# Kernel optimization log

Measured on AMD Instinct MI355X. Metric: run time of the kernel, lower is better.

The kernel has to match this reference:

```python
import jax, jax.numpy as jnp
import numpy as np

C = 256
RED = 8
CR = C // RED  # 32
B, H, W = 4, 64, 64
EPS = 1e-5


def setup_inputs() -> dict:
    key = jax.random.key(0)
    ks = jax.random.split(key, 12)
    s = 0.05
    return {
        "x": jax.random.normal(ks[0], (B, C, H, W), dtype=jnp.float32),
        "Wq": jax.random.normal(ks[1], (CR, C), dtype=jnp.float32) * s,
        "bq": jax.random.normal(ks[2], (CR,), dtype=jnp.float32) * s,
        "Wk": jax.random.normal(ks[3], (CR, C), dtype=jnp.float32) * s,
        "bk": jax.random.normal(ks[4], (CR,), dtype=jnp.float32) * s,
        "Wv": jax.random.normal(ks[5], (C, C), dtype=jnp.float32) * s,
        "bv": jax.random.normal(ks[6], (C,), dtype=jnp.float32) * s,
        "Wo": jax.random.normal(ks[7], (C, C), dtype=jnp.float32) * s,
        "bo": jax.random.normal(ks[8], (C,), dtype=jnp.float32) * s,
        "gamma": jnp.ones((C,), dtype=jnp.float32),
        "beta": jnp.zeros((C,), dtype=jnp.float32),
        "running_mean": jax.random.normal(ks[9], (C,), dtype=jnp.float32) * s,
        "running_var": jax.random.uniform(ks[10], (C,), dtype=jnp.float32, minval=0.5, maxval=1.5),
    }


def reference(x, Wq, bq, Wk, bk, Wv, bv, Wo, bo, gamma, beta, running_mean, running_var):
    b, c, h, w = x.shape
    n = h * w
    scale = c ** (-0.5)  # use_scale=True: in_channels**-0.5
    xf = x.reshape(b, c, n)  # [B, C, N]
    # 1x1 convs == per-pixel channel matmuls
    q = jnp.einsum('oc,bcn->bon', Wq, xf) + bq[None, :, None]   # [B, CR, N]
    k = jnp.einsum('oc,bcn->bon', Wk, xf) + bk[None, :, None]   # [B, CR, N]
    v = jnp.einsum('oc,bcn->bon', Wv, xf) + bv[None, :, None]   # [B, C, N]
    # attention[b, q_pos, k_pos], softmax over key positions (dim=2)
    attn = jnp.einsum('bcq,bck->bqk', q, k) * scale             # [B, N, N]
    attn = jax.nn.softmax(attn, axis=2)
    # out[b, c, q_pos] = sum_k v[b, c, k] * attn[b, q_pos, k]
    out = jnp.einsum('bck,bqk->bcq', v, attn)                   # [B, C, N]
    out = jnp.einsum('oc,bcn->bon', Wo, out) + bo[None, :, None]
    # BatchNorm2d (inference: running stats)
    inv = gamma / jnp.sqrt(running_var + EPS)
    out = out * inv[None, :, None] + (beta - running_mean * inv)[None, :, None]
    out = out.reshape(b, c, h, w)
    return jax.nn.relu(out + x)
```

## Files before the change

kernel.cpp:

```cpp
#include <hip/hip_runtime.h>
#include <hip/hip_bf16.h>

typedef unsigned short u16;
typedef unsigned int u32;

#define B_ 4
#define C_ 256
#define N_ 4096

constexpr float C1 = 0.09016844005556021f;

typedef float f32x16 __attribute__((ext_vector_type(16)));
typedef short bf16x8 __attribute__((ext_vector_type(8)));
typedef u32 u32x4 __attribute__((ext_vector_type(4)));
typedef int i32x2 __attribute__((ext_vector_type(2)));

__device__ __forceinline__ u16 bf16r(float f) {
    union { float f; u32 u; } a; a.f = f;
    u32 u = a.u;
    u += 0x7fffu + ((u >> 16) & 1u);
    return (u16)(u >> 16);
}

__device__ __forceinline__ float bf2f(u16 h) {
    union { u32 u; float f; } a; a.u = ((u32)h) << 16; return a.f;
}

__device__ __forceinline__ u32 pk2(float a, float b) {
    __hip_bfloat162 h = __float22bfloat162_rn(make_float2(a, b));
    union { __hip_bfloat162 h; u32 u; } c; c.h = h;
    return c.u;
}

__device__ __forceinline__ u32 cvtpk(float lo, float hi) {
    u32 r;
    asm("v_cvt_pk_bf16_f32 %0, %1, %2" : "=v"(r) : "v"(lo), "v"(hi));
    return r;
}

__device__ __forceinline__ void swap32(u32 &a, u32 &b) {
#if __has_builtin(__builtin_amdgcn_permlane32_swap)
    i32x2 r = __builtin_amdgcn_permlane32_swap((int)a, (int)b, false, false);
    a = (u32)r.x; b = (u32)r.y;
#else
    u32 as = __shfl_xor(a, 32), bs = __shfl_xor(b, 32);
    int hi = (threadIdx.x & 32) ? 1 : 0;
    u32 na = hi ? bs : a;
    u32 nb = hi ? b : as;
    a = na; b = nb;
#endif
}

__device__ __forceinline__ bf16x8 ld8(const u16* p) {
    return *reinterpret_cast<const bf16x8*>(p);
}

__device__ __forceinline__ void gld_lds16(const u16* g, u16* lbase, int lane) {
#if __has_builtin(__builtin_amdgcn_global_load_lds)
    __builtin_amdgcn_global_load_lds(
        (const __attribute__((address_space(1))) void*)g,
        (__attribute__((address_space(3))) void*)lbase, 16, 0, 0);
#else
    *reinterpret_cast<bf16x8*>(lbase + lane * 8) = ld8(g);
#endif
}

__device__ __forceinline__ int crow(int r, int hi) { return (r & 3) + 8 * (r >> 2) + 4 * hi; }

__global__ __launch_bounds__(256) void prep(
    const float* __restrict__ Wq, const float* __restrict__ Wk,
    const float* __restrict__ Wv, const float* __restrict__ Wo,
    const float* __restrict__ bo, const float* __restrict__ gamma,
    const float* __restrict__ beta, const float* __restrict__ rm, const float* __restrict__ rv,
    u16* __restrict__ wqk, u16* __restrict__ wv_b, u16* __restrict__ wo_b,
    float* __restrict__ scale, float* __restrict__ shift)
{
    int i = blockIdx.x * 256 + threadIdx.x;
    if (i < 16384) {
        float w = (i < 8192) ? Wq[i] * C1 : Wk[i - 8192];
        wqk[i] = bf16r(w);
    } else if (i < 81920) {
        wv_b[i - 16384] = bf16r(Wv[i - 16384]);
    } else if (i < 147456) {
        wo_b[i - 81920] = bf16r(Wo[i - 81920]);
    } else if (i < 147712) {
        int o = i - 147456;
        float inv = gamma[o] * rsqrtf(rv[o] + 1e-5f);
        scale[o] = inv;
        shift[o] = beta[o] + (bo[o] - rm[o]) * inv;
    }
}

__global__ __launch_bounds__(512) void projf(
    const float* __restrict__ x, const u16* __restrict__ wqk, const u16* __restrict__ wv,
    const float* __restrict__ bq, const float* __restrict__ bk, const float* __restrict__ bv,
    u16* __restrict__ qkt, u16* __restrict__ vout)
{
    __shared__ u16 xt[64 * 256];
    int tid = threadIdx.x;
    int lane = tid & 63, wid = tid >> 6;
    int r31 = lane & 31, hi = lane >> 5;
    int b = blockIdx.y, n0 = blockIdx.x * 64;
    const float* xb = x + (size_t)b * C_ * N_ + n0;
#pragma unroll
    for (int i = 0; i < 16; ++i) {
        int c2 = i * 8 + wid;
        int n = lane;
        float a0 = xb[(size_t)(2 * c2) * N_ + n];
        float a1 = xb[(size_t)(2 * c2 + 1) * N_ + n];
        int slot = (c2 >> 2) ^ (n & 31);
        *reinterpret_cast<u32*>(&xt[n * 256 + slot * 8 + (c2 & 3) * 2]) = pk2(a0, a1);
    }
    __syncthreads();
    for (int i = 0; i < 3; ++i) {
        int t = wid + i * 8;
        if (t < 20) {
            bool isqk = (t < 4);
            int nb = isqk ? (t >> 1) * 32 : ((t - 4) & 1) * 32;
            int gb = isqk ? (t & 1) * 32 : ((t - 4) >> 1) * 32;
            const u16* grow = (isqk ? wqk : wv) + (size_t)(gb + r31) * C_ + hi * 8;
            f32x16 acc;
#pragma unroll
            for (int r = 0; r < 16; ++r) acc[r] = 0.f;
#pragma unroll
            for (int ks = 0; ks < 16; ++ks) {
                int slot = (2 * ks + hi) ^ r31;
                bf16x8 lf = ld8(&xt[(nb + r31) * 256 + slot * 8]);
                bf16x8 gf = ld8(grow + ks * 16);
                if (isqk) acc = __builtin_amdgcn_mfma_f32_32x32x16_bf16(lf, gf, acc, 0, 0, 0);
                else      acc = __builtin_amdgcn_mfma_f32_32x32x16_bf16(gf, lf, acc, 0, 0, 0);
            }
            if (isqk) {
                int o = gb + r31;
                float bias = (o < 32) ? bq[o] * C1 : bk[o - 32];
                u16* qrow = qkt + ((size_t)b * N_ + n0 + nb) * 64 + o;
#pragma unroll
                for (int r = 0; r < 16; ++r)
                    qrow[(size_t)crow(r, hi) * 64] = bf16r(acc[r] + bias);
            } else {
                u16* vb = vout + (size_t)b * C_ * N_ + n0 + nb + r31;
#pragma unroll
                for (int r = 0; r < 16; ++r) {
                    int c = gb + crow(r, hi);
                    vb[(size_t)c * N_] = bf16r(acc[r] + bv[c]);
                }
            }
        }
    }
}

__global__ __launch_bounds__(512, 4) void attn(
    const u16* __restrict__ qkt, const u16* __restrict__ v,
    u16* __restrict__ opart, float* __restrict__ lpart, int kts)
{
    __shared__ u16 vt[2][128 * 128];
    __shared__ u16 ktt[2][16 * 128];
    int tid = threadIdx.x;
    int lane = tid & 63, wid = tid >> 6;
    int r31 = lane & 31, hi = lane >> 5;

    int nwg = 32 * 4 * gridDim.z;
    int wgl = blockIdx.x + 32 * (blockIdx.y + 4 * blockIdx.z);
    int cpx = nwg >> 3;
    int swzid = (wgl & 7) * cpx + (wgl >> 3);
    int bx = swzid & 31;
    int by = (swzid >> 5) & 3;
    int bz = swzid >> 7;

    int b = by, zs = bz;
    int q0 = bx * 128 + (wid >> 1) * 32;
    int cb = (wid & 1) * 128;
    const u16* qkb = qkt + (size_t)b * N_ * 64;
    const u16* vbase = v + (size_t)b * C_ * N_;

    int ks_q = tid & 255;
    int ks_row = ks_q >> 4;
    int ks_so = (ks_q & 15) ^ ks_row;
    int ks_k = ks_row * 4 + (ks_so >> 2);
    int ks_d8 = (ks_so & 3) * 8;

    int cpar8 = ((cb + r31) & 1) * 8;
    int vrow0 = (cb + r31) >> 1;
    int vm = vrow0 & 15;
    int kr4 = r31 >> 2;
    int kk3 = (r31 & 3) * 4;

    bf16x8 qf0 = ld8(qkb + (size_t)(q0 + r31) * 64 + hi * 8);
    bf16x8 qf1 = ld8(qkb + (size_t)(q0 + r31) * 64 + 16 + hi * 8);

    f32x16 acc[4];
#pragma unroll
    for (int ct = 0; ct < 4; ++ct)
#pragma unroll
        for (int r = 0; r < 16; ++r) acc[ct][r] = 0.f;

    f32x16 z4;
#pragma unroll
    for (int r = 0; r < 16; ++r) z4[r] = 0.f;

    float l_run = 0.f;
    int ktBeg = zs * kts, ktEnd = (zs + 1) * kts;

    auto stage = [&](int buf, int kt) {
        int k0 = kt * 64;
        if (tid < 256)
            gld_lds16(qkb + (size_t)(k0 + ks_k) * 64 + 32 + ks_d8,
                      &ktt[buf][(size_t)(wid * 64) * 8], lane);
#pragma unroll
        for (int i = 0; i < 4; ++i) {
            int q = i * 512 + tid;
            int row2 = q >> 4;
            int so = (q & 15) ^ (row2 & 15);
            int c = 2 * row2 + (so >> 3);
            int kcol = (so & 7) * 8;
            gld_lds16(vbase + (size_t)c * N_ + k0 + kcol,
                      &vt[buf][(size_t)((i * 512 + wid * 64) * 8)], lane);
        }
    };

    int cur = 0;
    stage(cur, ktBeg);
    __syncthreads();

    for (int kt = ktBeg; kt < ktEnd; ++kt) {
        if (kt + 1 < ktEnd) stage(cur ^ 1, kt + 1);

        float pst = 0.f;
#pragma unroll
        for (int ph = 0; ph < 2; ++ph) {
            int krow = ph * 8 + kr4;
            const u16* kbase = &ktt[cur][krow * 128];
            bf16x8 kf0 = ld8(kbase + (((kk3 + hi) ^ krow) * 8));
            bf16x8 kf1 = ld8(kbase + (((kk3 + 2 + hi) ^ krow) * 8));
            f32x16 s = __builtin_amdgcn_mfma_f32_32x32x16_bf16(kf0, qf0, z4, 0, 0, 0);
            s = __builtin_amdgcn_mfma_f32_32x32x16_bf16(kf1, qf1, s, 0, 0, 0);
            float p[16];
#pragma unroll
            for (int r = 0; r < 16; ++r) { p[r] = __builtin_amdgcn_exp2f(s[r]); pst += p[r]; }
            bf16x8 pf[2];
#pragma unroll
            for (int c16 = 0; c16 < 2; ++c16) {
                u32 w0 = cvtpk(p[8 * c16 + 0], p[8 * c16 + 1]);
                u32 w1 = cvtpk(p[8 * c16 + 2], p[8 * c16 + 3]);
                u32 w2 = cvtpk(p[8 * c16 + 4], p[8 * c16 + 5]);
                u32 w3 = cvtpk(p[8 * c16 + 6], p[8 * c16 + 7]);
                swap32(w0, w2);
                swap32(w1, w3);
                union { bf16x8 f8; u32 u[4]; } fu;
                fu.u[0] = w0; fu.u[1] = w1; fu.u[2] = w2; fu.u[3] = w3;
                pf[c16] = fu.f8;
            }
            int kc0 = ph * 2;
#pragma unroll
            for (int ct = 0; ct < 4; ++ct) {
                const u16* vb2 = &vt[cur][(vrow0 + 16 * ct) * 128];
                bf16x8 vf0 = ld8(vb2 + (((cpar8 + kc0 * 2 + hi) ^ vm) * 8));
                bf16x8 vf1 = ld8(vb2 + (((cpar8 + kc0 * 2 + 2 + hi) ^ vm) * 8));
                acc[ct] = __builtin_amdgcn_mfma_f32_32x32x16_bf16(vf0, pf[0], acc[ct], 0, 0, 0);
                acc[ct] = __builtin_amdgcn_mfma_f32_32x32x16_bf16(vf1, pf[1], acc[ct], 0, 0, 0);
            }
        }
        pst += __shfl_xor(pst, 32);
        l_run += pst;

        __syncthreads();
        cur ^= 1;
    }

    u16* dst = opart + ((size_t)(zs * B_ + b) * N_) * C_;
    if ((wid & 1) == 0 && hi == 0)
        lpart[((size_t)zs * B_ + b) * N_ + q0 + r31] = l_run;
    float (*tls)[32][33] = reinterpret_cast<float (*)[32][33]>(&vt[0][0]);
    int qg = lane >> 4, cd = lane & 15;
#pragma unroll
    for (int ct = 0; ct < 4; ++ct) {
        __syncthreads();
#pragma unroll
        for (int r = 0; r < 16; ++r)
            tls[wid][crow(r, hi)][r31] = acc[ct][r];
        __syncthreads();
#pragma unroll
        for (int it = 0; it < 8; ++it) {
            int qp = it * 4 + qg;
            u32 w = pk2(tls[wid][2 * cd][qp], tls[wid][2 * cd + 1][qp]);
            *reinterpret_cast<u32*>(dst + (size_t)(q0 + qp) * C_ + cb + ct * 32 + 2 * cd) = w;
        }
    }
}

__global__ __launch_bounds__(512) void outprojf(
    const u16* __restrict__ opart, const float* __restrict__ lpart,
    const u16* __restrict__ wo, const float* __restrict__ scl, const float* __restrict__ shf,
    const float* __restrict__ x, float* __restrict__ out, int S)
{
    __shared__ u16 ot[64 * 256];
    __shared__ float linv[64];
    int tid = threadIdx.x;
    int lane = tid & 63, wid = tid >> 6;
    int r31 = lane & 31, hi = lane >> 5;
    int b = blockIdx.y, n0 = blockIdx.x * 64;
    if (tid < 64) {
        float l = 0.f;
        for (int s = 0; s < S; ++s) l += lpart[((size_t)s * B_ + b) * N_ + n0 + tid];
        linv[tid] = 1.f / l;
    }
    __syncthreads();
#pragma unroll
    for (int i = 0; i < 4; ++i) {
        int chunk = i * 512 + tid;
        int n = chunk >> 5, c8 = chunk & 31;
        float a[8];
#pragma unroll
        for (int j = 0; j < 8; ++j) a[j] = 0.f;
        for (int s = 0; s < S; ++s) {
            bf16x8 o = ld8(opart + (((size_t)s * B_ + b) * N_ + n0 + n) * C_ + c8 * 8);
#pragma unroll
            for (int j = 0; j < 8; ++j) a[j] += bf2f((u16)o[j]);
        }
        float li = linv[n];
        u32x4 w;
#pragma unroll
        for (int j = 0; j < 4; ++j) w[j] = pk2(a[2 * j] * li, a[2 * j + 1] * li);
        int sws = c8 ^ (n & 31);
        *reinterpret_cast<u32x4*>(&ot[n * 256 + sws * 8]) = w;
    }
    __syncthreads();
    int obs = wid * 32;
    const u16* arow = wo + (size_t)(obs + r31) * C_ + hi * 8;
    f32x16 acc0, acc1;
#pragma unroll
    for (int r = 0; r < 16; ++r) { acc0[r] = 0.f; acc1[r] = 0.f; }
#pragma unroll
    for (int ks = 0; ks < 16; ++ks) {
        bf16x8 af = ld8(arow + ks * 16);
        int slot = (2 * ks + hi) ^ r31;
        bf16x8 b0 = ld8(&ot[r31 * 256 + slot * 8]);
        bf16x8 b1 = ld8(&ot[(32 + r31) * 256 + slot * 8]);
        acc0 = __builtin_amdgcn_mfma_f32_32x32x16_bf16(af, b0, acc0, 0, 0, 0);
        acc1 = __builtin_amdgcn_mfma_f32_32x32x16_bf16(af, b1, acc1, 0, 0, 0);
    }
    const float* xb = x + (size_t)b * C_ * N_;
    float* op = out + (size_t)b * C_ * N_;
#pragma unroll
    for (int r = 0; r < 16; ++r) {
        int o = obs + crow(r, hi);
        float sc = scl[o], sh = shf[o];
        size_t base = (size_t)o * N_ + n0;
        float v0 = acc0[r] * sc + sh + xb[base + r31];
        op[base + r31] = fmaxf(v0, 0.f);
        float v1 = acc1[r] * sc + sh + xb[base + 32 + r31];
        op[base + 32 + r31] = fmaxf(v1, 0.f);
    }
}

extern "C" void kernel_launch(void* const* d_in, const int* in_sizes, int n_in,
                              void* d_out, int out_size, void* d_ws, size_t ws_size,
                              hipStream_t stream) {
    const float* x     = (const float*)d_in[0];
    const float* Wq    = (const float*)d_in[1];
    const float* bq    = (const float*)d_in[2];
    const float* Wk    = (const float*)d_in[3];
    const float* bk    = (const float*)d_in[4];
    const float* Wv    = (const float*)d_in[5];
    const float* bv    = (const float*)d_in[6];
    const float* Wo    = (const float*)d_in[7];
    const float* bo    = (const float*)d_in[8];
    const float* gamma = (const float*)d_in[9];
    const float* beta  = (const float*)d_in[10];
    const float* rmean = (const float*)d_in[11];
    const float* rvar  = (const float*)d_in[12];
    float* out = (float*)d_out;

    char* ws = (char*)d_ws;
    u16* vbuf = (u16*)(ws);
    u16* qkt  = (u16*)(ws + (size_t)(8u << 20));
    char* wsm = ws + (size_t)(10u << 20);
    u16* wqk  = (u16*)(wsm);
    u16* wv_b = (u16*)(wsm + 32768);
    u16* wo_b = (u16*)(wsm + 32768 + 131072);
    float* scl = (float*)(wsm + 32768 + 262144);
    float* shf = scl + 256;
    float* lpart = (float*)(ws + (size_t)(11u << 20));
    u16* opart = (u16*)(ws + (size_t)(12u << 20));

    size_t need4 = (size_t)(12u << 20) + 4 * (size_t)(8u << 20);
    size_t need2 = (size_t)(12u << 20) + 2 * (size_t)(8u << 20);
    int S = (ws_size >= need4) ? 4 : (ws_size >= need2) ? 2 : 1;

    prep<<<dim3(578), dim3(256), 0, stream>>>(Wq, Wk, Wv, Wo, bo, gamma, beta, rmean, rvar,
                                              wqk, wv_b, wo_b, scl, shf);
    projf<<<dim3(64, 4), dim3(512), 0, stream>>>(x, wqk, wv_b, bq, bk, bv, qkt, vbuf);
    attn<<<dim3(32, 4, S), dim3(512), 0, stream>>>(qkt, vbuf, opart, lpart, 64 / S);
    outprojf<<<dim3(64, 4), dim3(512), 0, stream>>>(opart, lpart, wo_b, scl, shf, x, out, S);
}
```

Measured before the change: 85.69 us.

## Give each attention wave all channels, halving block size and dropping duplicate QK

Result: faster. 81.72 us (-4.6%).

```diff
diff --git a/kernel.cpp b/kernel.cpp
--- a/kernel.cpp
+++ b/kernel.cpp
@@ -149,7 +149,7 @@
     }
 }
 
-__global__ __launch_bounds__(512, 4) void attn(
+__global__ __launch_bounds__(256, 2) void attn(
     const u16* __restrict__ qkt, const u16* __restrict__ v,
     u16* __restrict__ opart, float* __restrict__ lpart, int kts)
 {
@@ -168,29 +168,26 @@
     int bz = swzid >> 7;
 
     int b = by, zs = bz;
-    int q0 = bx * 128 + (wid >> 1) * 32;
-    int cb = (wid & 1) * 128;
+    int q0 = bx * 128 + wid * 32;
     const u16* qkb = qkt + (size_t)b * N_ * 64;
     const u16* vbase = v + (size_t)b * C_ * N_;
 
-    int ks_q = tid & 255;
-    int ks_row = ks_q >> 4;
-    int ks_so = (ks_q & 15) ^ ks_row;
+    int ks_row = tid >> 4;
+    int ks_so = (tid & 15) ^ ks_row;
     int ks_k = ks_row * 4 + (ks_so >> 2);
     int ks_d8 = (ks_so & 3) * 8;
 
-    int cpar8 = ((cb + r31) & 1) * 8;
-    int vrow0 = (cb + r31) >> 1;
-    int vm = vrow0 & 15;
+    int cpar8 = (r31 & 1) * 8;
+    int vrow0 = r31 >> 1;
     int kr4 = r31 >> 2;
     int kk3 = (r31 & 3) * 4;
 
     bf16x8 qf0 = ld8(qkb + (size_t)(q0 + r31) * 64 + hi * 8);
     bf16x8 qf1 = ld8(qkb + (size_t)(q0 + r31) * 64 + 16 + hi * 8);
 
-    f32x16 acc[4];
-#pragma unroll
-    for (int ct = 0; ct < 4; ++ct)
+    f32x16 acc[8];
+#pragma unroll
+    for (int ct = 0; ct < 8; ++ct)
 #pragma unroll
         for (int r = 0; r < 16; ++r) acc[ct][r] = 0.f;
 
@@ -203,18 +200,17 @@
 
     auto stage = [&](int buf, int kt) {
         int k0 = kt * 64;
-        if (tid < 256)
-            gld_lds16(qkb + (size_t)(k0 + ks_k) * 64 + 32 + ks_d8,
-                      &ktt[buf][(size_t)(wid * 64) * 8], lane);
-#pragma unroll
-        for (int i = 0; i < 4; ++i) {
-            int q = i * 512 + tid;
+        gld_lds16(qkb + (size_t)(k0 + ks_k) * 64 + 32 + ks_d8,
+                  &ktt[buf][(size_t)(wid * 64) * 8], lane);
+#pragma unroll
+        for (int i = 0; i < 8; ++i) {
+            int q = i * 256 + tid;
             int row2 = q >> 4;
             int so = (q & 15) ^ (row2 & 15);
             int c = 2 * row2 + (so >> 3);
             int kcol = (so & 7) * 8;
             gld_lds16(vbase + (size_t)c * N_ + k0 + kcol,
-                      &vt[buf][(size_t)((i * 512 + wid * 64) * 8)], lane);
+                      &vt[buf][(size_t)((i * 256 + wid * 64) * 8)], lane);
         }
     };
 
@@ -225,18 +221,19 @@
     for (int kt = ktBeg; kt < ktEnd; ++kt) {
         if (kt + 1 < ktEnd) stage(cur ^ 1, kt + 1);
 
-        float pst = 0.f;
 #pragma unroll
         for (int ph = 0; ph < 2; ++ph) {
             int krow = ph * 8 + kr4;
             const u16* kbase = &ktt[cur][krow * 128];
             bf16x8 kf0 = ld8(kbase + (((kk3 + hi) ^ krow) * 8));
             bf16x8 kf1 = ld8(kbase + (((kk3 + 2 + hi) ^ krow) * 8));
+            __builtin_amdgcn_s_setprio(1);
             f32x16 s = __builtin_amdgcn_mfma_f32_32x32x16_bf16(kf0, qf0, z4, 0, 0, 0);
             s = __builtin_amdgcn_mfma_f32_32x32x16_bf16(kf1, qf1, s, 0, 0, 0);
+            __builtin_amdgcn_s_setprio(0);
             float p[16];
 #pragma unroll
-            for (int r = 0; r < 16; ++r) { p[r] = __builtin_amdgcn_exp2f(s[r]); pst += p[r]; }
+            for (int r = 0; r < 16; ++r) { p[r] = __builtin_amdgcn_exp2f(s[r]); l_run += p[r]; }
             bf16x8 pf[2];
 #pragma unroll
             for (int c16 = 0; c16 < 2; ++c16) {
@@ -251,29 +248,31 @@
                 pf[c16] = fu.f8;
             }
             int kc0 = ph * 2;
-#pragma unroll
-            for (int ct = 0; ct < 4; ++ct) {
+            __builtin_amdgcn_s_setprio(1);
+#pragma unroll
+            for (int ct = 0; ct < 8; ++ct) {
                 const u16* vb2 = &vt[cur][(vrow0 + 16 * ct) * 128];
-                bf16x8 vf0 = ld8(vb2 + (((cpar8 + kc0 * 2 + hi) ^ vm) * 8));
-                bf16x8 vf1 = ld8(vb2 + (((cpar8 + kc0 * 2 + 2 + hi) ^ vm) * 8));
+                bf16x8 vf0 = ld8(vb2 + (((cpar8 + kc0 * 2 + hi) ^ vrow0) * 8));
+                bf16x8 vf1 = ld8(vb2 + (((cpar8 + kc0 * 2 + 2 + hi) ^ vrow0) * 8));
                 acc[ct] = __builtin_amdgcn_mfma_f32_32x32x16_bf16(vf0, pf[0], acc[ct], 0, 0, 0);
                 acc[ct] = __builtin_amdgcn_mfma_f32_32x32x16_bf16(vf1, pf[1], acc[ct], 0, 0, 0);
             }
-        }
-        pst += __shfl_xor(pst, 32);
-        l_run += pst;
+            __builtin_amdgcn_s_setprio(0);
+        }
 
         __syncthreads();
         cur ^= 1;
     }
 
+    l_run += __shfl_xor(l_run, 32);
+
     u16* dst = opart + ((size_t)(zs * B_ + b) * N_) * C_;
-    if ((wid & 1) == 0 && hi == 0)
+    if (hi == 0)
         lpart[((size_t)zs * B_ + b) * N_ + q0 + r31] = l_run;
     float (*tls)[32][33] = reinterpret_cast<float (*)[32][33]>(&vt[0][0]);
     int qg = lane >> 4, cd = lane & 15;
 #pragma unroll
-    for (int ct = 0; ct < 4; ++ct) {
+    for (int ct = 0; ct < 8; ++ct) {
         __syncthreads();
 #pragma unroll
         for (int r = 0; r < 16; ++r)
@@ -283,7 +282,7 @@
         for (int it = 0; it < 8; ++it) {
             int qp = it * 4 + qg;
             u32 w = pk2(tls[wid][2 * cd][qp], tls[wid][2 * cd + 1][qp]);
-            *reinterpret_cast<u32*>(dst + (size_t)(q0 + qp) * C_ + cb + ct * 32 + 2 * cd) = w;
+            *reinterpret_cast<u32*>(dst + (size_t)(q0 + qp) * C_ + ct * 32 + 2 * cd) = w;
         }
     }
 }
@@ -390,6 +389,6 @@
     prep<<<dim3(578), dim3(256), 0, stream>>>(Wq, Wk, Wv, Wo, bo, gamma, beta, rmean, rvar,
                                               wqk, wv_b, wo_b, scl, shf);
     projf<<<dim3(64, 4), dim3(512), 0, stream>>>(x, wqk, wv_b, bq, bk, bv, qkt, vbuf);
-    attn<<<dim3(32, 4, S), dim3(512), 0, stream>>>(qkt, vbuf, opart, lpart, 64 / S);
+    attn<<<dim3(32, 4, S), dim3(256), 0, stream>>>(qkt, vbuf, opart, lpart, 64 / S);
     outprojf<<<dim3(64, 4), dim3(512), 0, stream>>>(opart, lpart, wo_b, scl, shf, x, out, S);
 }
```
